# Kernel optimization log

Measured on AMD Instinct MI355X. Metric: run time of the kernel, lower is better.

Reference implementation:

```python
import jax, jax.numpy as jnp
import numpy as np

NEG = -1000000.0


def setup_inputs() -> dict:
    key = jax.random.key(0)
    k0, k1, k2, k3, k4 = jax.random.split(key, 5)
    b, c, h, w = 4, 256, 64, 64
    dvt_c = 768
    x = jax.random.normal(k0, (b, c, h, w), jnp.float32)
    dvtfeats = jax.random.normal(k1, (b, dvt_c, h, w), jnp.float32)
    coarse = (jax.random.uniform(k2, (b, 1, h, w)) > 0.5).astype(jnp.float32)
    mask = jnp.repeat(jnp.repeat(coarse, 8, axis=2), 8, axis=3)  # [b,1,512,512]
    # K_conv: Conv2d(c+768 -> c, 1x1) with bias; fuse: Conv2d(2c -> c, 1x1) no bias
    K_w = jax.random.normal(k3, (c, c + dvt_c), jnp.float32) * 0.02
    K_b = jnp.zeros((c,), jnp.float32)
    fuse_w = jax.random.normal(k4, (c, 2 * c), jnp.float32) * 0.02
    return {"x": x, "mask": mask, "dvtfeats": dvtfeats, "K_w": K_w, "K_b": K_b, "fuse_w": fuse_w}


def _conv1x1(inp, w, b=None):
    out = jnp.einsum('bihw,oi->bohw', inp, w)
    if b is not None:
        out = out + b[None, :, None, None]
    return out


def _forward(x, mask, dvtfeats, K_w, K_b, fuse_w):
    b, c, h, w = x.shape
    n = h * w
    # maxpool(8,8) then binarize
    m = mask.reshape(b, 1, h, 8, w, 8).max(axis=(3, 5))
    m = (m > 0).astype(x.dtype)            # [b,1,h,w] foreground mask
    bm = 1.0 - m                            # background mask
    # K_conv applied once (original applies the same conv twice to the same input)
    feats = _conv1x1(jnp.concatenate([x, dvtfeats], axis=1), K_w, K_b)  # [b,c,h,w]
    K = (feats * bm).reshape(b, c, n)
    Q = (feats * m).reshape(b, c, n).transpose(0, 2, 1)  # [b,n,c]
    K = K / (jnp.linalg.norm(K, axis=1, keepdims=True) + 1e-8)
    Q = Q / (jnp.linalg.norm(Q, axis=2, keepdims=True) + 1e-8)
    V = (x * bm).reshape(b, c, n)
    score = jnp.einsum('bqc,bck->bqk', Q, K) * 20.0       # [b,n,n] cosine sims
    qm = m.reshape(b, 1, n)    # query mask (foreground)
    km = bm.reshape(b, 1, n)   # key mask (background)
    score = score + (1.0 - km) * NEG + (1.0 - qm).transpose(0, 2, 1) * NEG
    att = jax.nn.softmax(score, axis=-1)
    att = att * qm.transpose(0, 2, 1) * km                # zero out invalid rows/cols
    # att_fore[b,c,q] = sum_k V[b,c,k] * att[b,q,k]
    att_fore = jnp.einsum('bck,bqk->bcq', V, att).reshape(b, c, h, w)
    fused = _conv1x1(jnp.concatenate([att_fore, x], axis=1), fuse_w)
    visatt = att.sum(axis=1).reshape(b, 1, h, w)          # sum over query dim
    attmask = jnp.repeat(jnp.repeat(visatt, 8, axis=2), 8, axis=3)  # nearest upsample x8
    attmask = attmask / attmask.max()
    out = fused * m + x * (1.0 - m)
    return out, attmask


def reference(x, mask, dvtfeats, K_w, K_b, fuse_w):
    return _forward(x, mask, dvtfeats, K_w, K_b, fuse_w)
```

## Files before the change

kernel.cpp:

```cpp
#include <hip/hip_runtime.h>
#include <hip/hip_bf16.h>

typedef __attribute__((ext_vector_type(8))) short short8;
typedef __attribute__((ext_vector_type(4))) float f32x4;
typedef unsigned int uint;
typedef unsigned short ushort;

constexpr int BATCH = 4;
constexpr int CH    = 256;
constexpr int N     = 4096;
constexpr int DVC   = 768;
constexpr int CIN   = 1024;
constexpr int KC    = 512;
constexpr int PBS   = 5 * 1024 * 1024;
constexpr int QCH   = 32;
constexpr int SPLITK = 4;

constexpr size_t OFF_M    = 0;
constexpr size_t OFF_INV  = 64ull << 10;
constexpr size_t OFF_VIS  = 128ull << 10;
constexpr size_t OFF_MAXV = 192ull << 10;
constexpr size_t OFF_CNT  = 196ull << 10;
constexpr size_t OFF_FGI  = 256ull << 10;
constexpr size_t OFF_BGI  = 320ull << 10;
constexpr size_t OFF_P2S  = 384ull << 10;
constexpr size_t OFF_KMC  = 448ull << 10;
constexpr size_t OFF_PART = 1ull << 20;
constexpr size_t OFF_KWB  = 5ull << 20;
constexpr size_t OFF_FWB  = OFF_KWB + (512ull << 10);
constexpr size_t OFF_XT   = 6ull << 20;
constexpr size_t OFF_QC   = 38ull << 20;
constexpr size_t OFF_KCC  = 46ull << 20;
constexpr size_t OFF_XC   = 54ull << 20;
constexpr size_t OFF_AFT  = 62ull << 20;
constexpr size_t OFF_P    = 70ull << 20;
constexpr size_t OFF_AFP  = 110ull << 20;

__device__ __forceinline__ ushort f2bf(float f) {
    __hip_bfloat16 h = __float2bfloat16(f);
    return __builtin_bit_cast(ushort, h);
}
__device__ __forceinline__ float bf2f(ushort u) {
    uint v = (uint)u << 16;
    return __builtin_bit_cast(float, v);
}

typedef const __attribute__((address_space(1))) uint* gptr_t;
typedef __attribute__((address_space(3))) uint* lptr_t;
__device__ __forceinline__ void gload_lds16(const void* g, void* l) {
    __builtin_amdgcn_global_load_lds((gptr_t)g, (lptr_t)l, 16, 0, 0);
}

template<int WM, int WN>
__device__ __forceinline__ void gemm_core(
    const ushort* __restrict__ A0, int lda, int m0,
    const ushort* __restrict__ B0, int ldb0, int kend0,
    const ushort* __restrict__ B1, int ldb1,
    int n0, int K,
    ushort* AsL, ushort* BsL, f32x4 acc[4][4])
{
    constexpr int NW = WM * WN, BM = WM * 64, BN = WN * 64;
    const int t = threadIdx.x, lane = t & 63, wid = t >> 6;
    const int wm = (wid / WN) * 64, wn = (wid % WN) * 64;

    for (int k0 = 0; k0 < K; k0 += 64) {
        #pragma unroll
        for (int c = wid; c < BM / 8; c += NW) {
            const ushort* g = A0 + (size_t)(m0 + c * 8 + (lane >> 3)) * lda + (k0 + (lane & 7) * 8);
            gload_lds16(g, AsL + c * 512);
        }
        const ushort* Bsrc = (k0 < kend0) ? B0 : B1;
        const int ldb = (k0 < kend0) ? ldb0 : ldb1;
        const int kc  = (k0 < kend0) ? k0 : (k0 - kend0);
        #pragma unroll
        for (int c = wid; c < BN / 8; c += NW) {
            const ushort* g = Bsrc + (size_t)(n0 + c * 8 + (lane >> 3)) * ldb + (kc + (lane & 7) * 8);
            gload_lds16(g, BsL + c * 512);
        }
        __syncthreads();

        const int ra = wm + (lane & 15), rb = wn + (lane & 15), ko = (lane >> 4) * 8;
        #pragma unroll
        for (int kk = 0; kk < 64; kk += 32) {
            short8 a[4], b[4];
            #pragma unroll
            for (int i = 0; i < 4; i++) a[i] = *(const short8*)(AsL + (ra + i * 16) * 64 + kk + ko);
            #pragma unroll
            for (int j = 0; j < 4; j++) b[j] = *(const short8*)(BsL + (rb + j * 16) * 64 + kk + ko);
            #pragma unroll
            for (int i = 0; i < 4; i++)
                #pragma unroll
                for (int j = 0; j < 4; j++)
                    acc[i][j] = __builtin_amdgcn_mfma_f32_16x16x32_bf16(a[i], b[j], acc[i][j], 0, 0, 0);
        }
        __syncthreads();
    }
}

__device__ __forceinline__ void zero_acc(f32x4 acc[4][4]) {
    f32x4 z = {0.f, 0.f, 0.f, 0.f};
    #pragma unroll
    for (int i = 0; i < 4; i++)
        #pragma unroll
        for (int j = 0; j < 4; j++) acc[i][j] = z;
}

__global__ void k_prep(const float* __restrict__ mask, const float* __restrict__ Kw,
                       const float* __restrict__ fw, float* __restrict__ m,
                       float* __restrict__ vis, uint* __restrict__ maxv,
                       ushort* __restrict__ Kwb, ushort* __restrict__ fwb)
{
    const int bid = blockIdx.x;
    if (bid < 64) {
        int idx = bid * 256 + threadIdx.x;
        int b = idx >> 12, p = idx & 4095;
        int y = p >> 6, x = p & 63;
        const float* base = mask + (size_t)b * 512 * 512 + (y * 8) * 512 + x * 8;
        float mx = 0.f;
        for (int dy = 0; dy < 8; dy++) {
            #pragma unroll
            for (int dx = 0; dx < 8; dx++) mx = fmaxf(mx, base[dy * 512 + dx]);
        }
        m[idx] = (mx > 0.f) ? 1.f : 0.f;
        vis[idx] = 0.f;
        if (idx == 0) maxv[0] = 0u;
    } else {
        int i = (bid - 64) * 256 + threadIdx.x;
        if (i < CH * CIN) Kwb[i] = f2bf(Kw[i]);
        else              fwb[i - CH * CIN] = f2bf(fw[i - CH * CIN]);
    }
}

__global__ __launch_bounds__(256) void k_scan(
    const float* __restrict__ m, int* __restrict__ fgi, int* __restrict__ bgi,
    int* __restrict__ counts, float* __restrict__ kmc, int* __restrict__ p2s)
{
    const int b = blockIdx.x, t = threadIdx.x;
    const float* mb = m + (size_t)b * N;
    __shared__ int sfg[256], sbg[256];
    bool isf[16];
    int cf = 0, cb_ = 0;
    #pragma unroll
    for (int j = 0; j < 16; j++) {
        bool f = mb[t * 16 + j] != 0.f;
        isf[j] = f; cf += f ? 1 : 0; cb_ += f ? 0 : 1;
    }
    sfg[t] = cf; sbg[t] = cb_;
    __syncthreads();
    for (int off = 1; off < 256; off <<= 1) {
        int vf = (t >= off) ? sfg[t - off] : 0;
        int vb = (t >= off) ? sbg[t - off] : 0;
        __syncthreads();
        sfg[t] += vf; sbg[t] += vb;
        __syncthreads();
    }
    int basef = sfg[t] - cf, baseb = sbg[t] - cb_;
    int nfg = sfg[255], nbg = sbg[255];
    #pragma unroll
    for (int j = 0; j < 16; j++) {
        int p = t * 16 + j;
        if (isf[j]) { fgi[b * N + basef] = p; p2s[b * N + p] = basef | (1 << 30); basef++; }
        else        { bgi[b * N + baseb] = p; p2s[b * N + p] = baseb; baseb++; }
    }
    if (t == 0) {
        counts[b * 4 + 0] = nfg;
        counts[b * 4 + 1] = (nfg + 127) & ~127;
        counts[b * 4 + 2] = nbg;
        counts[b * 4 + 3] = (nbg + 127) & ~127;
    }
    for (int j = t; j < N; j += 256) kmc[b * N + j] = (j < nbg) ? 1.f : 0.f;
}

__global__ __launch_bounds__(256) void k_tr(const float* __restrict__ src,
                                            ushort* __restrict__ dst, int C)
{
    __shared__ float Ls[64][65];
    const int ci0 = blockIdx.x * 64, n0 = blockIdx.y * 64, b = blockIdx.z;
    const float* s = src + (size_t)b * C * 4096;
    const int t = threadIdx.x;
    #pragma unroll
    for (int it = 0; it < 4; it++) {
        int f4 = it * 256 + t;
        int r = f4 >> 4, c4 = f4 & 15;
        float4 v = *(const float4*)(s + (size_t)(ci0 + r) * 4096 + n0 + c4 * 4);
        Ls[r][c4 * 4 + 0] = v.x; Ls[r][c4 * 4 + 1] = v.y;
        Ls[r][c4 * 4 + 2] = v.z; Ls[r][c4 * 4 + 3] = v.w;
    }
    __syncthreads();
    ushort* d = dst + (size_t)b * 4096 * C;
    #pragma unroll
    for (int it = 0; it < 8; it++) {
        int p = it * 256 + t;
        int rn = p >> 5, cc2 = p & 31;
        uint val = (uint)f2bf(Ls[cc2 * 2][rn]) | ((uint)f2bf(Ls[cc2 * 2 + 1][rn]) << 16);
        *(uint*)(d + (size_t)(n0 + rn) * C + ci0 + cc2 * 2) = val;
    }
}

__global__ __launch_bounds__(256) void k_vgather(
    const ushort* __restrict__ xT, const int* __restrict__ bgi,
    const int* __restrict__ counts, ushort* __restrict__ xc)
{
    __shared__ ushort Xs[64][264];
    const int b = blockIdx.y;
    const int ki0 = blockIdx.x * 64;
    const int nbg = counts[b * 4 + 2], nbgp = counts[b * 4 + 3];
    if (ki0 >= nbgp) return;
    const int t = threadIdx.x;
    const int j = t >> 2, part = t & 3;
    const int ki = ki0 + j;
    if (ki < nbg) {
        const ushort* src = xT + ((size_t)b * N + bgi[(size_t)b * N + ki]) * CH + part * 64;
        #pragma unroll
        for (int q = 0; q < 8; q++)
            *(uint4*)&Xs[j][part * 64 + q * 8] = *(const uint4*)(src + q * 8);
    } else {
        uint4 z = {0, 0, 0, 0};
        #pragma unroll
        for (int q = 0; q < 8; q++)
            *(uint4*)&Xs[j][part * 64 + q * 8] = z;
    }
    __syncthreads();
    const int c = t;
    ushort* dst = xc + ((size_t)b * CH + c) * N + ki0;
    uint w[32];
    #pragma unroll
    for (int jj = 0; jj < 32; jj++)
        w[jj] = (uint)Xs[2 * jj][c] | ((uint)Xs[2 * jj + 1][c] << 16);
    #pragma unroll
    for (int q = 0; q < 8; q++) {
        uint4 o = { w[q * 4], w[q * 4 + 1], w[q * 4 + 2], w[q * 4 + 3] };
        *(uint4*)(dst + q * 8) = o;
    }
}

__global__ __launch_bounds__(256) void k_feats(
    const ushort* __restrict__ Kwb, const ushort* __restrict__ xT,
    const float* __restrict__ dvt, const float* __restrict__ Kb,
    const int* __restrict__ p2s, ushort* __restrict__ Qc, ushort* __restrict__ Kc)
{
    __shared__ ushort As[256 * 64];
    __shared__ ushort Bs[32 * 64];
    __shared__ float  Ls[64][33];
    __shared__ float  red[4][32];
    const int b = blockIdx.z;
    const int n0 = blockIdx.x * 32;
    const int t = threadIdx.x, lane = t & 63, wid = t >> 6;
    const ushort* xTb = xT + (size_t)b * N * CH;
    const float* dvb = dvt + (size_t)b * DVC * N;
    f32x4 acc[4][2];
    {
        f32x4 z = {0.f, 0.f, 0.f, 0.f};
        #pragma unroll
        for (int i = 0; i < 4; i++) { acc[i][0] = z; acc[i][1] = z; }
    }

    for (int k0 = 0; k0 < 256; k0 += 64) {
        #pragma unroll
        for (int c = wid; c < 32; c += 4)
            gload_lds16(Kwb + (size_t)(c * 8 + (lane >> 3)) * CIN + k0 + (lane & 7) * 8, As + c * 512);
        gload_lds16(xTb + (size_t)(n0 + wid * 8 + (lane >> 3)) * CH + k0 + (lane & 7) * 8, Bs + wid * 512);
        __syncthreads();
        const int ra = wid * 64 + (lane & 15), rb = lane & 15, ko = (lane >> 4) * 8;
        #pragma unroll
        for (int kk = 0; kk < 64; kk += 32) {
            short8 a[4], bb[2];
            #pragma unroll
            for (int i = 0; i < 4; i++) a[i] = *(const short8*)(As + (ra + i * 16) * 64 + kk + ko);
            #pragma unroll
            for (int j = 0; j < 2; j++) bb[j] = *(const short8*)(Bs + (rb + j * 16) * 64 + kk + ko);
            #pragma unroll
            for (int i = 0; i < 4; i++)
                #pragma unroll
                for (int j = 0; j < 2; j++)
                    acc[i][j] = __builtin_amdgcn_mfma_f32_16x16x32_bf16(a[i], bb[j], acc[i][j], 0, 0, 0);
        }
        __syncthreads();
    }
    for (int k0 = 256; k0 < 1024; k0 += 64) {
        #pragma unroll
        for (int c = wid; c < 32; c += 4)
            gload_lds16(Kwb + (size_t)(c * 8 + (lane >> 3)) * CIN + k0 + (lane & 7) * 8, As + c * 512);
        const float* dsrc = dvb + (size_t)(k0 - 256) * N + n0;
        #pragma unroll
        for (int it = 0; it < 2; it++) {
            int f4 = it * 256 + t;
            int r = f4 >> 3, c4 = (f4 & 7) * 4;
            float4 v = *(const float4*)(dsrc + (size_t)r * N + c4);
            Ls[r][c4 + 0] = v.x; Ls[r][c4 + 1] = v.y;
            Ls[r][c4 + 2] = v.z; Ls[r][c4 + 3] = v.w;
        }
        __syncthreads();
        {
            int rn = t & 31;
            int ks = (t >> 5) * 8;
            #pragma unroll
            for (int j2 = 0; j2 < 4; j2++) {
                int kk = ks + j2 * 2;
                uint val = (uint)f2bf(Ls[kk][rn]) | ((uint)f2bf(Ls[kk + 1][rn]) << 16);
                int idx = (rn * 64 + kk) ^ ((rn & 7) << 3);
                *(uint*)(Bs + idx) = val;
            }
        }
        __syncthreads();
        const int ra = wid * 64 + (lane & 15), rb = lane & 15, ko = (lane >> 4) * 8;
        #pragma unroll
        for (int kk = 0; kk < 64; kk += 32) {
            short8 a[4], bb[2];
            #pragma unroll
            for (int i = 0; i < 4; i++) a[i] = *(const short8*)(As + (ra + i * 16) * 64 + kk + ko);
            #pragma unroll
            for (int j = 0; j < 2; j++) {
                int row = rb + j * 16;
                int idx = (row * 64 + kk + ko) ^ ((row & 7) << 3);
                bb[j] = *(const short8*)(Bs + idx);
            }
            #pragma unroll
            for (int i = 0; i < 4; i++)
                #pragma unroll
                for (int j = 0; j < 2; j++)
                    acc[i][j] = __builtin_amdgcn_mfma_f32_16x16x32_bf16(a[i], bb[j], acc[i][j], 0, 0, 0);
        }
        __syncthreads();
    }

    const int wm = wid * 64;
    float sj[2] = {0.f, 0.f};
    #pragma unroll
    for (int i = 0; i < 4; i++) {
        int mbase = wm + i * 16 + ((lane >> 4) * 4);
        float4 bias = *(const float4*)(Kb + mbase);
        #pragma unroll
        for (int j = 0; j < 2; j++) {
            acc[i][j][0] += bias.x; acc[i][j][1] += bias.y;
            acc[i][j][2] += bias.z; acc[i][j][3] += bias.w;
            sj[j] += acc[i][j][0] * acc[i][j][0] + acc[i][j][1] * acc[i][j][1]
                   + acc[i][j][2] * acc[i][j][2] + acc[i][j][3] * acc[i][j][3];
        }
    }
    #pragma unroll
    for (int j = 0; j < 2; j++) {
        sj[j] += __shfl_xor(sj[j], 16);
        sj[j] += __shfl_xor(sj[j], 32);
    }
    if (lane < 16) {
        red[wid][lane]      = sj[0];
        red[wid][16 + lane] = sj[1];
    }
    __syncthreads();
    const int* pb = p2s + (size_t)b * N + n0;
    #pragma unroll
    for (int j = 0; j < 2; j++) {
        int n = j * 16 + (lane & 15);
        float s = red[0][n] + red[1][n] + red[2][n] + red[3][n];
        float invn = 1.f / (sqrtf(s) + 1e-8f);
        int sl = pb[n];
        ushort* dst = (sl & (1 << 30)) ? Qc : Kc;
        int slot = sl & 0x3FFFFFFF;
        ushort* drow = dst + ((size_t)b * N + slot) * CH;
        #pragma unroll
        for (int i = 0; i < 4; i++) {
            int mbase = wm + i * 16 + ((lane >> 4) * 4);
            ushort4 o = { f2bf(acc[i][j][0] * invn), f2bf(acc[i][j][1] * invn),
                          f2bf(acc[i][j][2] * invn), f2bf(acc[i][j][3] * invn) };
            *(ushort4*)(drow + mbase) = o;
        }
    }
}

__global__ __launch_bounds__(128) void k_score(
    const ushort* __restrict__ Qc, const ushort* __restrict__ Kc,
    const float* __restrict__ kmc, const int* __restrict__ counts,
    ushort* __restrict__ P, float* __restrict__ rowpart)
{
    const int b = blockIdx.z;
    const int nfgp = counts[b * 4 + 1], nbgp = counts[b * 4 + 3];
    const int m0 = blockIdx.y * 128;
    const int n0 = blockIdx.x * 64;
    if (m0 >= nfgp || n0 >= nbgp) return;
    __shared__ ushort SH[(128 + 64) * 64];
    const int t = threadIdx.x, lane = t & 63, wid = t >> 6;
    const ushort* Qb = Qc + (size_t)b * N * CH;
    const ushort* Kb_ = Kc + (size_t)b * N * CH;
    f32x4 acc[4][4]; zero_acc(acc);
    gemm_core<2, 1>(Qb, CH, m0, Kb_, CH, CH, Kb_, CH, n0, CH, SH, SH + 128 * 64, acc);

    const int wm = wid * 64;
    float km[4];
    #pragma unroll
    for (int j = 0; j < 4; j++) km[j] = kmc[(size_t)b * N + n0 + j * 16 + (lane & 15)];

    ushort* Cs = SH;
    float sir[4][4] = {};
    #pragma unroll
    for (int i = 0; i < 4; i++) {
        int rbase = wm + i * 16 + ((lane >> 4) * 4);
        #pragma unroll
        for (int j = 0; j < 4; j++) {
            int cl = j * 16 + (lane & 15);
            #pragma unroll
            for (int r = 0; r < 4; r++) {
                float p = (km[j] != 0.f) ? __expf(20.f * acc[i][j][r] - 20.f) : 0.f;
                Cs[(rbase + r) * 64 + cl] = f2bf(p);
                sir[i][r] += p;
            }
        }
    }
    #pragma unroll
    for (int i = 0; i < 4; i++)
        #pragma unroll
        for (int r = 0; r < 4; r++) {
            float s = sir[i][r];
            s += __shfl_xor(s, 1); s += __shfl_xor(s, 2);
            s += __shfl_xor(s, 4); s += __shfl_xor(s, 8);
            sir[i][r] = s;
        }
    if ((lane & 15) == 0) {
        float* rp = rowpart + (size_t)(n0 >> 6) * (BATCH * N) + (size_t)b * N + m0;
        #pragma unroll
        for (int i = 0; i < 4; i++)
            #pragma unroll
            for (int r = 0; r < 4; r++)
                rp[wm + i * 16 + ((lane >> 4) * 4) + r] = sir[i][r];
    }
    __syncthreads();
    ushort* Pb = P + (size_t)b * PBS;
    #pragma unroll
    for (int it = 0; it < 8; it++) {
        int v8 = it * 128 + t;
        int row = v8 >> 3, c8 = (v8 & 7) * 8;
        *(uint4*)(Pb + (size_t)(m0 + row) * nbgp + n0 + c8) = *(const uint4*)(Cs + row * 64 + c8);
    }
}

__global__ void k_rowinv(const float* __restrict__ rowpart, const int* __restrict__ counts,
                         float* __restrict__ inv)
{
    int g = blockIdx.x * 256 + threadIdx.x;
    int b = g >> 12, qi = g & 4095;
    int nfgp = counts[b * 4 + 1], nbgp = counts[b * 4 + 3];
    if (qi >= nfgp) return;
    int nsl = nbgp >> 6;
    float s = 0.f;
    for (int sl = 0; sl < nsl; sl++) s += rowpart[(size_t)sl * (BATCH * N) + g];
    inv[g] = (s > 0.f) ? 1.f / s : 0.f;
}

__global__ __launch_bounds__(256) void k_att_fore(
    const ushort* __restrict__ xc, const ushort* __restrict__ P,
    const int* __restrict__ counts, ushort* __restrict__ AFp)
{
    const int b = blockIdx.z & (BATCH - 1);
    const int sk = blockIdx.z / BATCH;
    const int nfgp = counts[b * 4 + 1], nbgp = counts[b * 4 + 3];
    const int n0 = blockIdx.x * 64;
    if (n0 >= nfgp) return;
    const int kchunk = ((nbgp / 64 + SPLITK - 1) / SPLITK) * 64;
    const int k0s = sk * kchunk;
    const int len = min(kchunk, nbgp - k0s);

    const int lane = threadIdx.x & 63, wid = threadIdx.x >> 6;
    f32x4 acc[4][4]; zero_acc(acc);
    if (len > 0) {
        __shared__ ushort SH[(256 + 64) * 64];
        const ushort* Pb = P + (size_t)b * PBS + k0s;
        gemm_core<4, 1>(xc + (size_t)b * CH * N + k0s, N, 0,
                        Pb, nbgp, 1 << 30, Pb, nbgp,
                        n0, len, SH, SH + 256 * 64, acc);
    }
    ushort* Ap = AFp + ((size_t)(sk * BATCH + b) * N) * CH;
    const int wm = wid * 64;
    #pragma unroll
    for (int j = 0; j < 4; j++) {
        int qi = n0 + j * 16 + (lane & 15);
        #pragma unroll
        for (int i = 0; i < 4; i++) {
            int mbase = wm + i * 16 + ((lane >> 4) * 4);
            ushort4 o = { f2bf(acc[i][j][0]), f2bf(acc[i][j][1]),
                          f2bf(acc[i][j][2]), f2bf(acc[i][j][3]) };
            *(ushort4*)(Ap + (size_t)qi * CH + mbase) = o;
        }
    }
}

__global__ __launch_bounds__(256) void k_afreduce(
    const ushort* __restrict__ AFp, const float* __restrict__ inv,
    const int* __restrict__ fgi, const int* __restrict__ counts,
    ushort* __restrict__ AFt)
{
    const int t = threadIdx.x, lane = t & 63, wid = t >> 6;
    const int g = blockIdx.x * 4 + wid;
    const int b = g >> 12, qi = g & 4095;
    if (qi >= counts[b * 4]) return;
    const size_t rowoff = ((size_t)b * N + qi) * CH + lane * 4;
    float s0 = 0.f, s1 = 0.f, s2 = 0.f, s3 = 0.f;
    #pragma unroll
    for (int sk = 0; sk < SPLITK; sk++) {
        ushort4 v = *(const ushort4*)(AFp + (size_t)sk * BATCH * N * CH + rowoff);
        s0 += bf2f(v.x); s1 += bf2f(v.y); s2 += bf2f(v.z); s3 += bf2f(v.w);
    }
    float iq = inv[g];
    int q = fgi[g];
    ushort4 o = { f2bf(s0 * iq), f2bf(s1 * iq), f2bf(s2 * iq), f2bf(s3 * iq) };
    *(ushort4*)(AFt + ((size_t)b * N + q) * CH + lane * 4) = o;
}

__global__ __launch_bounds__(128) void k_fused(
    const ushort* __restrict__ fwb, const ushort* __restrict__ AFt,
    const ushort* __restrict__ xT, const float* __restrict__ x,
    const float* __restrict__ m_, float* __restrict__ out)
{
    __shared__ ushort SH[(64 + 128) * 64];
    const int b = blockIdx.z;
    const int n0 = blockIdx.x * 128, m0 = blockIdx.y * 64;
    const int lane = threadIdx.x & 63, wid = threadIdx.x >> 6;
    const int wn = (wid & 1) * 64;
    f32x4 acc[4][4]; zero_acc(acc);
    gemm_core<1, 2>(fwb, KC, m0,
                    AFt + (size_t)b * N * CH, CH, CH,
                    xT + (size_t)b * N * CH, CH,
                    n0, KC, SH, SH + 64 * 64, acc);
    const float* mb = m_ + (size_t)b * N;
    const float* xc_ = x + (size_t)b * CH * N;
    float* ob = out + (size_t)b * CH * N;
    #pragma unroll
    for (int j = 0; j < 4; j++) {
        int n = n0 + wn + j * 16 + (lane & 15);
        float mv = mb[n];
        #pragma unroll
        for (int i = 0; i < 4; i++) {
            int mbase = m0 + i * 16 + ((lane >> 4) * 4);
            #pragma unroll
            for (int r = 0; r < 4; r++) {
                int c = mbase + r;
                ob[(size_t)c * N + n] = (mv != 0.f) ? acc[i][j][r] : xc_[(size_t)c * N + n];
            }
        }
    }
}

__global__ __launch_bounds__(256) void k_colsum(
    const ushort* __restrict__ P, const float* __restrict__ inv,
    const int* __restrict__ counts, float* __restrict__ part)
{
    const int b = blockIdx.z, qc = blockIdx.y, t = threadIdx.x;
    const int nfg = counts[b * 4], nbgp = counts[b * 4 + 3];
    const int ki0 = blockIdx.x * 2048 + t * 8;
    if (ki0 >= nbgp) return;
    const int qchunk = (nfg + QCH - 1) / QCH;
    const int q0 = qc * qchunk, q1 = min(q0 + qchunk, nfg);
    const ushort* base = P + (size_t)b * PBS + (size_t)q0 * nbgp + ki0;
    const float* ib = inv + (size_t)b * N;
    float acc[8] = {};
    int q = q0;
    for (; q + 4 <= q1; q += 4) {
        uint4 v0 = *(const uint4*)(base);
        uint4 v1 = *(const uint4*)(base + (size_t)nbgp);
        uint4 v2 = *(const uint4*)(base + 2 * (size_t)nbgp);
        uint4 v3 = *(const uint4*)(base + 3 * (size_t)nbgp);
        float i0 = ib[q], i1 = ib[q + 1], i2 = ib[q + 2], i3 = ib[q + 3];
        const ushort* u0 = (const ushort*)&v0;
        const ushort* u1 = (const ushort*)&v1;
        const ushort* u2 = (const ushort*)&v2;
        const ushort* u3 = (const ushort*)&v3;
        #pragma unroll
        for (int e = 0; e < 8; e++)
            acc[e] += bf2f(u0[e]) * i0 + bf2f(u1[e]) * i1 + bf2f(u2[e]) * i2 + bf2f(u3[e]) * i3;
        base += 4 * (size_t)nbgp;
    }
    for (; q < q1; q++) {
        uint4 v = *(const uint4*)(base);
        float iq = ib[q];
        const ushort* u = (const ushort*)&v;
        #pragma unroll
        for (int e = 0; e < 8; e++) acc[e] += bf2f(u[e]) * iq;
        base += (size_t)nbgp;
    }
    float* pp = part + (size_t)qc * (BATCH * N) + (size_t)b * N + ki0;
    float4 o0 = {acc[0], acc[1], acc[2], acc[3]};
    float4 o1 = {acc[4], acc[5], acc[6], acc[7]};
    *(float4*)(pp)     = o0;
    *(float4*)(pp + 4) = o1;
}

__global__ void k_colsum_final(const float* __restrict__ part, const int* __restrict__ bgi,
                               const int* __restrict__ counts, float* __restrict__ vis,
                               uint* __restrict__ maxv)
{
    int g = blockIdx.x * 256 + threadIdx.x;
    int b = g >> 12, ki = g & 4095;
    int t = threadIdx.x;
    float s = 0.f;
    if (ki < counts[b * 4 + 2]) {
        #pragma unroll
        for (int j = 0; j < QCH; j++) s += part[(size_t)j * (BATCH * N) + g];
        vis[(size_t)b * N + bgi[(size_t)b * N + ki]] = s;
    }
    __shared__ float red[256];
    red[t] = s; __syncthreads();
    for (int st = 128; st > 0; st >>= 1) { if (t < st) red[t] = fmaxf(red[t], red[t + st]); __syncthreads(); }
    if (t == 0) atomicMax(maxv, __float_as_uint(red[0]));
}

__global__ void k_attmask(const float* __restrict__ vis, const float* __restrict__ maxv,
                          float* __restrict__ amask)
{
    int idx = blockIdx.x * 256 + threadIdx.x;
    int b = idx >> 18;
    int r = idx & 262143;
    int Y = r >> 9, X = r & 511;
    amask[idx] = vis[(size_t)b * N + (Y >> 3) * 64 + (X >> 3)] / maxv[0];
}

extern "C" void kernel_launch(void* const* d_in, const int* in_sizes, int n_in,
                              void* d_out, int out_size, void* d_ws, size_t ws_size,
                              hipStream_t stream)
{
    const float* x    = (const float*)d_in[0];
    const float* mask = (const float*)d_in[1];
    const float* dvt  = (const float*)d_in[2];
    const float* Kw   = (const float*)d_in[3];
    const float* Kb   = (const float*)d_in[4];
    const float* fw   = (const float*)d_in[5];
    float* out = (float*)d_out;

    char* ws = (char*)d_ws;
    float*  m    = (float*)(ws + OFF_M);
    float*  inv  = (float*)(ws + OFF_INV);
    float*  vis  = (float*)(ws + OFF_VIS);
    float*  maxv = (float*)(ws + OFF_MAXV);
    int*    cnt  = (int*)  (ws + OFF_CNT);
    int*    fgi  = (int*)  (ws + OFF_FGI);
    int*    bgi  = (int*)  (ws + OFF_BGI);
    int*    p2s  = (int*)  (ws + OFF_P2S);
    float*  kmc  = (float*)(ws + OFF_KMC);
    float*  part = (float*)(ws + OFF_PART);
    ushort* Kwb  = (ushort*)(ws + OFF_KWB);
    ushort* fwb  = (ushort*)(ws + OFF_FWB);
    ushort* xT   = (ushort*)(ws + OFF_XT);
    ushort* Qc   = (ushort*)(ws + OFF_QC);
    ushort* Kcc  = (ushort*)(ws + OFF_KCC);
    ushort* xc   = (ushort*)(ws + OFF_XC);
    ushort* AFt  = (ushort*)(ws + OFF_AFT);
    ushort* P    = (ushort*)(ws + OFF_P);
    ushort* AFp  = (ushort*)(ws + OFF_AFP);

    k_prep       <<<dim3(64 + (CH * CIN + CH * KC) / 256), 256, 0, stream>>>(
                     mask, Kw, fw, m, vis, (uint*)maxv, Kwb, fwb);
    k_scan       <<<dim3(BATCH), 256, 0, stream>>>(m, fgi, bgi, cnt, kmc, p2s);
    k_tr         <<<dim3(CH / 64, 64, BATCH), 256, 0, stream>>>(x, xT, CH);
    k_feats      <<<dim3(N / 32, 1, BATCH), 256, 0, stream>>>(Kwb, xT, dvt, Kb, p2s, Qc, Kcc);
    k_vgather    <<<dim3(N / 64, BATCH), 256, 0, stream>>>(xT, bgi, cnt, xc);
    k_score      <<<dim3(N / 64, N / 128, BATCH), 128, 0, stream>>>(Qc, Kcc, kmc, cnt, P, part);
    k_rowinv     <<<dim3(BATCH * N / 256), 256, 0, stream>>>(part, cnt, inv);
    k_att_fore   <<<dim3(N / 64, 1, BATCH * SPLITK), 256, 0, stream>>>(xc, P, cnt, AFp);
    k_afreduce   <<<dim3(BATCH * N / 4), 256, 0, stream>>>(AFp, inv, fgi, cnt, AFt);
    k_colsum     <<<dim3(2, QCH, BATCH), 256, 0, stream>>>(P, inv, cnt, part);
    k_colsum_final<<<dim3(BATCH * N / 256), 256, 0, stream>>>(part, bgi, cnt, vis, (uint*)maxv);
    k_fused      <<<dim3(N / 128, CH / 64, BATCH), 128, 0, stream>>>(fwb, AFt, xT, x, m, out);
    k_attmask    <<<dim3(BATCH * 512 * 512 / 256), 256, 0, stream>>>(vis, maxv, out + (size_t)BATCH * CH * N);
}
```

Baseline: 170.9 us.

## Fuse score, row-normalization and attention-value GEMM into one flash-style kernel

Replaces the separate score, row-inverse, split-K att_fore and reduction kernels with a single kernel. Each 32-query block streams 64-key tiles, computes exp scores, accumulates row sums in shared memory, and multiplies by the V tile on the fly. Normalization and the scatter to AFt happen at the end. This removes the P read-back, the AFp partial buffers and several launches. In exchange it uses small 32-query blocks with no split-K, which gives fewer blocks per batch and many syncthreads per tile with no double buffering. P is still written because the column sum needs it.

```diff
diff --git a/kernel.cpp b/kernel.cpp
--- a/kernel.cpp
+++ b/kernel.cpp
@@ -14,7 +14,6 @@
 constexpr int KC    = 512;
 constexpr int PBS   = 5 * 1024 * 1024;
 constexpr int QCH   = 32;
-constexpr int SPLITK = 4;
 
 constexpr size_t OFF_M    = 0;
 constexpr size_t OFF_INV  = 64ull << 10;
@@ -34,7 +33,6 @@
 constexpr size_t OFF_XC   = 54ull << 20;
 constexpr size_t OFF_AFT  = 62ull << 20;
 constexpr size_t OFF_P    = 70ull << 20;
-constexpr size_t OFF_AFP  = 110ull << 20;
 
 __device__ __forceinline__ ushort f2bf(float f) {
     __hip_bfloat16 h = __float2bfloat16(f);
@@ -368,141 +366,135 @@
     }
 }
 
-__global__ __launch_bounds__(128) void k_score(
+__global__ __launch_bounds__(256) void k_attn(
     const ushort* __restrict__ Qc, const ushort* __restrict__ Kc,
-    const float* __restrict__ kmc, const int* __restrict__ counts,
-    ushort* __restrict__ P, float* __restrict__ rowpart)
-{
-    const int b = blockIdx.z;
-    const int nfgp = counts[b * 4 + 1], nbgp = counts[b * 4 + 3];
-    const int m0 = blockIdx.y * 128;
-    const int n0 = blockIdx.x * 64;
-    if (m0 >= nfgp || n0 >= nbgp) return;
-    __shared__ ushort SH[(128 + 64) * 64];
+    const ushort* __restrict__ xc, const float* __restrict__ kmc,
+    const int* __restrict__ fgi, const int* __restrict__ counts,
+    ushort* __restrict__ P, float* __restrict__ inv, ushort* __restrict__ AFt)
+{
+    const int b = blockIdx.y;
+    const int n0 = blockIdx.x * 32;
+    const int nfg = counts[b * 4], nfgp = counts[b * 4 + 1], nbgp = counts[b * 4 + 3];
+    if (n0 >= nfgp) return;
+    __shared__ ushort Qs[32 * 256];
+    __shared__ ushort SH[64 * 256];
+    __shared__ ushort Ps[32 * 64];
+    __shared__ float  rs[4][32];
+    __shared__ float  invs[32];
     const int t = threadIdx.x, lane = t & 63, wid = t >> 6;
-    const ushort* Qb = Qc + (size_t)b * N * CH;
-    const ushort* Kb_ = Kc + (size_t)b * N * CH;
-    f32x4 acc[4][4]; zero_acc(acc);
-    gemm_core<2, 1>(Qb, CH, m0, Kb_, CH, CH, Kb_, CH, n0, CH, SH, SH + 128 * 64, acc);
-
-    const int wm = wid * 64;
-    float km[4];
-    #pragma unroll
-    for (int j = 0; j < 4; j++) km[j] = kmc[(size_t)b * N + n0 + j * 16 + (lane & 15)];
-
-    ushort* Cs = SH;
-    float sir[4][4] = {};
-    #pragma unroll
-    for (int i = 0; i < 4; i++) {
-        int rbase = wm + i * 16 + ((lane >> 4) * 4);
-        #pragma unroll
-        for (int j = 0; j < 4; j++) {
-            int cl = j * 16 + (lane & 15);
+
+    const ushort* Qb = Qc + ((size_t)b * N + n0) * CH;
+    #pragma unroll
+    for (int c = wid; c < 16; c += 4)
+        gload_lds16(Qb + (size_t)(c * 2 + (lane >> 5)) * CH + (lane & 31) * 8, Qs + c * 512);
+    if (lane < 32) rs[wid][lane] = 0.f;
+    __syncthreads();
+
+    short8 qf[8][2];
+    #pragma unroll
+    for (int kc = 0; kc < 8; kc++)
+        #pragma unroll
+        for (int i = 0; i < 2; i++)
+            qf[kc][i] = *(const short8*)(Qs + (size_t)(i * 16 + (lane & 15)) * 256 + kc * 32 + (lane >> 4) * 8);
+
+    f32x4 acc_o[4][2];
+    { f32x4 z = {0.f,0.f,0.f,0.f};
+      #pragma unroll
+      for (int i = 0; i < 4; i++) { acc_o[i][0] = z; acc_o[i][1] = z; } }
+
+    const ushort* Kcb = Kc + (size_t)b * N * CH;
+    const ushort* xcb = xc + (size_t)b * CH * N;
+    ushort* Pb = P + (size_t)b * PBS;
+    const int kq = wid * 16;
+    const int nsteps = nbgp >> 6;
+
+    for (int s = 0; s < nsteps; s++) {
+        const int k0s = s * 64;
+        __syncthreads();
+        #pragma unroll
+        for (int c = wid; c < 32; c += 4)
+            gload_lds16(Kcb + (size_t)(k0s + c * 2 + (lane >> 5)) * CH + (lane & 31) * 8, SH + c * 512);
+        __syncthreads();
+
+        f32x4 acc_s[2];
+        { f32x4 z = {0.f,0.f,0.f,0.f}; acc_s[0] = z; acc_s[1] = z; }
+        #pragma unroll
+        for (int kc = 0; kc < 8; kc++) {
+            short8 bk = *(const short8*)(SH + (size_t)(kq + (lane & 15)) * 256 + kc * 32 + (lane >> 4) * 8);
+            acc_s[0] = __builtin_amdgcn_mfma_f32_16x16x32_bf16(qf[kc][0], bk, acc_s[0], 0, 0, 0);
+            acc_s[1] = __builtin_amdgcn_mfma_f32_16x16x32_bf16(qf[kc][1], bk, acc_s[1], 0, 0, 0);
+        }
+        __syncthreads();
+        #pragma unroll
+        for (int c = wid; c < 32; c += 4)
+            gload_lds16(xcb + (size_t)(c * 8 + (lane >> 3)) * N + k0s + (lane & 7) * 8, SH + c * 512);
+
+        float km = kmc[(size_t)b * N + k0s + kq + (lane & 15)];
+        #pragma unroll
+        for (int i = 0; i < 2; i++) {
+            float rsum[4];
             #pragma unroll
             for (int r = 0; r < 4; r++) {
-                float p = (km[j] != 0.f) ? __expf(20.f * acc[i][j][r] - 20.f) : 0.f;
-                Cs[(rbase + r) * 64 + cl] = f2bf(p);
-                sir[i][r] += p;
+                float p = (km != 0.f) ? __expf(20.f * acc_s[i][r] - 20.f) : 0.f;
+                int q = i * 16 + (lane >> 4) * 4 + r;
+                Ps[q * 64 + kq + (lane & 15)] = f2bf(p);
+                float ss = p;
+                ss += __shfl_xor(ss, 1); ss += __shfl_xor(ss, 2);
+                ss += __shfl_xor(ss, 4); ss += __shfl_xor(ss, 8);
+                rsum[r] = ss;
             }
-        }
-    }
-    #pragma unroll
-    for (int i = 0; i < 4; i++)
-        #pragma unroll
-        for (int r = 0; r < 4; r++) {
-            float s = sir[i][r];
-            s += __shfl_xor(s, 1); s += __shfl_xor(s, 2);
-            s += __shfl_xor(s, 4); s += __shfl_xor(s, 8);
-            sir[i][r] = s;
-        }
-    if ((lane & 15) == 0) {
-        float* rp = rowpart + (size_t)(n0 >> 6) * (BATCH * N) + (size_t)b * N + m0;
-        #pragma unroll
-        for (int i = 0; i < 4; i++)
-            #pragma unroll
-            for (int r = 0; r < 4; r++)
-                rp[wm + i * 16 + ((lane >> 4) * 4) + r] = sir[i][r];
+            if ((lane & 15) == 0) {
+                #pragma unroll
+                for (int r = 0; r < 4; r++)
+                    rs[wid][i * 16 + (lane >> 4) * 4 + r] += rsum[r];
+            }
+        }
+        __syncthreads();
+        {
+            int row = t >> 3, c8 = (t & 7) * 8;
+            *(uint4*)(Pb + (size_t)(n0 + row) * nbgp + k0s + c8) = *(const uint4*)(Ps + row * 64 + c8);
+        }
+        #pragma unroll
+        for (int kc2 = 0; kc2 < 2; kc2++) {
+            short8 av[4], bp[2];
+            #pragma unroll
+            for (int i = 0; i < 4; i++)
+                av[i] = *(const short8*)(SH + (size_t)(wid * 64 + i * 16 + (lane & 15)) * 64 + kc2 * 32 + (lane >> 4) * 8);
+            #pragma unroll
+            for (int j = 0; j < 2; j++)
+                bp[j] = *(const short8*)(Ps + (size_t)(j * 16 + (lane & 15)) * 64 + kc2 * 32 + (lane >> 4) * 8);
+            #pragma unroll
+            for (int i = 0; i < 4; i++)
+                #pragma unroll
+                for (int j = 0; j < 2; j++)
+                    acc_o[i][j] = __builtin_amdgcn_mfma_f32_16x16x32_bf16(av[i], bp[j], acc_o[i][j], 0, 0, 0);
+        }
     }
     __syncthreads();
-    ushort* Pb = P + (size_t)b * PBS;
-    #pragma unroll
-    for (int it = 0; it < 8; it++) {
-        int v8 = it * 128 + t;
-        int row = v8 >> 3, c8 = (v8 & 7) * 8;
-        *(uint4*)(Pb + (size_t)(m0 + row) * nbgp + n0 + c8) = *(const uint4*)(Cs + row * 64 + c8);
-    }
-}
-
-__global__ void k_rowinv(const float* __restrict__ rowpart, const int* __restrict__ counts,
-                         float* __restrict__ inv)
-{
-    int g = blockIdx.x * 256 + threadIdx.x;
-    int b = g >> 12, qi = g & 4095;
-    int nfgp = counts[b * 4 + 1], nbgp = counts[b * 4 + 3];
-    if (qi >= nfgp) return;
-    int nsl = nbgp >> 6;
-    float s = 0.f;
-    for (int sl = 0; sl < nsl; sl++) s += rowpart[(size_t)sl * (BATCH * N) + g];
-    inv[g] = (s > 0.f) ? 1.f / s : 0.f;
-}
-
-__global__ __launch_bounds__(256) void k_att_fore(
-    const ushort* __restrict__ xc, const ushort* __restrict__ P,
-    const int* __restrict__ counts, ushort* __restrict__ AFp)
-{
-    const int b = blockIdx.z & (BATCH - 1);
-    const int sk = blockIdx.z / BATCH;
-    const int nfgp = counts[b * 4 + 1], nbgp = counts[b * 4 + 3];
-    const int n0 = blockIdx.x * 64;
-    if (n0 >= nfgp) return;
-    const int kchunk = ((nbgp / 64 + SPLITK - 1) / SPLITK) * 64;
-    const int k0s = sk * kchunk;
-    const int len = min(kchunk, nbgp - k0s);
-
-    const int lane = threadIdx.x & 63, wid = threadIdx.x >> 6;
-    f32x4 acc[4][4]; zero_acc(acc);
-    if (len > 0) {
-        __shared__ ushort SH[(256 + 64) * 64];
-        const ushort* Pb = P + (size_t)b * PBS + k0s;
-        gemm_core<4, 1>(xc + (size_t)b * CH * N + k0s, N, 0,
-                        Pb, nbgp, 1 << 30, Pb, nbgp,
-                        n0, len, SH, SH + 256 * 64, acc);
-    }
-    ushort* Ap = AFp + ((size_t)(sk * BATCH + b) * N) * CH;
-    const int wm = wid * 64;
-    #pragma unroll
-    for (int j = 0; j < 4; j++) {
+    if (t < 32) {
+        float ssum = rs[0][t] + rs[1][t] + rs[2][t] + rs[3][t];
+        float iv = (ssum > 0.f) ? 1.f / ssum : 0.f;
+        invs[t] = iv;
+        inv[(size_t)b * N + n0 + t] = iv;
+    }
+    __syncthreads();
+    const int* fb = fgi + (size_t)b * N;
+    #pragma unroll
+    for (int j = 0; j < 2; j++) {
         int qi = n0 + j * 16 + (lane & 15);
-        #pragma unroll
-        for (int i = 0; i < 4; i++) {
-            int mbase = wm + i * 16 + ((lane >> 4) * 4);
-            ushort4 o = { f2bf(acc[i][j][0]), f2bf(acc[i][j][1]),
-                          f2bf(acc[i][j][2]), f2bf(acc[i][j][3]) };
-            *(ushort4*)(Ap + (size_t)qi * CH + mbase) = o;
-        }
-    }
-}
-
-__global__ __launch_bounds__(256) void k_afreduce(
-    const ushort* __restrict__ AFp, const float* __restrict__ inv,
-    const int* __restrict__ fgi, const int* __restrict__ counts,
-    ushort* __restrict__ AFt)
-{
-    const int t = threadIdx.x, lane = t & 63, wid = t >> 6;
-    const int g = blockIdx.x * 4 + wid;
-    const int b = g >> 12, qi = g & 4095;
-    if (qi >= counts[b * 4]) return;
-    const size_t rowoff = ((size_t)b * N + qi) * CH + lane * 4;
-    float s0 = 0.f, s1 = 0.f, s2 = 0.f, s3 = 0.f;
-    #pragma unroll
-    for (int sk = 0; sk < SPLITK; sk++) {
-        ushort4 v = *(const ushort4*)(AFp + (size_t)sk * BATCH * N * CH + rowoff);
-        s0 += bf2f(v.x); s1 += bf2f(v.y); s2 += bf2f(v.z); s3 += bf2f(v.w);
-    }
-    float iq = inv[g];
-    int q = fgi[g];
-    ushort4 o = { f2bf(s0 * iq), f2bf(s1 * iq), f2bf(s2 * iq), f2bf(s3 * iq) };
-    *(ushort4*)(AFt + ((size_t)b * N + q) * CH + lane * 4) = o;
+        if (qi < nfg) {
+            float iq = invs[j * 16 + (lane & 15)];
+            int qp = fb[qi];
+            ushort* Ab = AFt + ((size_t)b * N + qp) * CH;
+            #pragma unroll
+            for (int i = 0; i < 4; i++) {
+                int mbase = wid * 64 + i * 16 + (lane >> 4) * 4;
+                ushort4 o = { f2bf(acc_o[i][j][0] * iq), f2bf(acc_o[i][j][1] * iq),
+                              f2bf(acc_o[i][j][2] * iq), f2bf(acc_o[i][j][3] * iq) };
+                *(ushort4*)(Ab + mbase) = o;
+            }
+        }
+    }
 }
 
 __global__ __launch_bounds__(128) void k_fused(
@@ -643,7 +635,6 @@
     ushort* xc   = (ushort*)(ws + OFF_XC);
     ushort* AFt  = (ushort*)(ws + OFF_AFT);
     ushort* P    = (ushort*)(ws + OFF_P);
-    ushort* AFp  = (ushort*)(ws + OFF_AFP);
 
     k_prep       <<<dim3(64 + (CH * CIN + CH * KC) / 256), 256, 0, stream>>>(
                      mask, Kw, fw, m, vis, (uint*)maxv, Kwb, fwb);
@@ -651,10 +642,7 @@
     k_tr         <<<dim3(CH / 64, 64, BATCH), 256, 0, stream>>>(x, xT, CH);
     k_feats      <<<dim3(N / 32, 1, BATCH), 256, 0, stream>>>(Kwb, xT, dvt, Kb, p2s, Qc, Kcc);
     k_vgather    <<<dim3(N / 64, BATCH), 256, 0, stream>>>(xT, bgi, cnt, xc);
-    k_score      <<<dim3(N / 64, N / 128, BATCH), 128, 0, stream>>>(Qc, Kcc, kmc, cnt, P, part);
-    k_rowinv     <<<dim3(BATCH * N / 256), 256, 0, stream>>>(part, cnt, inv);
-    k_att_fore   <<<dim3(N / 64, 1, BATCH * SPLITK), 256, 0, stream>>>(xc, P, cnt, AFp);
-    k_afreduce   <<<dim3(BATCH * N / 4), 256, 0, stream>>>(AFp, inv, fgi, cnt, AFt);
+    k_attn       <<<dim3(N / 32, BATCH), 256, 0, stream>>>(Qc, Kcc, xc, kmc, fgi, cnt, P, inv, AFt);
     k_colsum     <<<dim3(2, QCH, BATCH), 256, 0, stream>>>(P, inv, cnt, part);
     k_colsum_final<<<dim3(BATCH * N / 256), 256, 0, stream>>>(part, bgi, cnt, vis, (uint*)maxv);
     k_fused      <<<dim3(N / 128, CH / 64, BATCH), 128, 0, stream>>>(fwb, AFt, xT, x, m, out);
```

After: 216.7 us. 1.27x slower.
